# Kernel optimization log

Hardware: AMD Instinct MI355X
Metric: run time of the kernel (lower is better)

The kernel has to match this reference:

```python
import jax, jax.numpy as jnp
import numpy as np

N_BINS = 15


def setup_inputs() -> dict:
    key = jax.random.key(0)
    k1, k2 = jax.random.split(key)
    N, C = 2_000_000, 100
    logits = jax.random.normal(k1, (N, C), dtype=jnp.float32)
    labels = jax.random.randint(k2, (N,), 0, C, dtype=jnp.int64)
    return {"logits": logits, "labels": labels}


def reference(logits, labels):
    # softmax confidences + predictions
    probs = jax.nn.softmax(logits, axis=1)
    conf = jnp.max(probs, axis=1)            # [N]
    pred = jnp.argmax(probs, axis=1)          # [N]
    acc = (pred == labels).astype(conf.dtype)  # [N]

    # torch loop uses bins (lower, upper] with boundaries linspace(0,1,16).
    # conf in ((b-1)/B, b/B] maps to bin b-1 == ceil(conf*B)-1 (clipped).
    bin_idx = jnp.clip(jnp.ceil(conf * N_BINS).astype(jnp.int32) - 1, 0, N_BINS - 1)

    counts = jax.ops.segment_sum(jnp.ones_like(conf), bin_idx, num_segments=N_BINS)
    sum_conf = jax.ops.segment_sum(conf, bin_idx, num_segments=N_BINS)
    sum_acc = jax.ops.segment_sum(acc, bin_idx, num_segments=N_BINS)

    nonempty = counts > 0
    safe = jnp.where(nonempty, counts, jnp.ones_like(counts))
    gap = jnp.abs(sum_conf / safe - sum_acc / safe)  # |avg_conf - acc| per bin

    n_total = jnp.asarray(conf.shape[0], conf.dtype)
    ece = jnp.sum(jnp.where(nonempty, gap * counts / n_total, 0.0))
    mce = jnp.max(jnp.where(nonempty, gap, -jnp.inf))
    mce = jnp.where(jnp.any(nonempty), mce, jnp.asarray(1.0, conf.dtype))
    return ece, mce
```

## Files before the change

### kernel.cpp

```cpp
#include <hip/hip_runtime.h>
#include <math.h>

#define NBINS 15

template<int CTRL>
__device__ __forceinline__ float dpp_f(float x) {
    return __int_as_float(__builtin_amdgcn_update_dpp(
        0, __float_as_int(x), CTRL, 0xF, 0xF, true));
}
template<int CTRL>
__device__ __forceinline__ int dpp_i(int x) {
    return __builtin_amdgcn_update_dpp(0, x, CTRL, 0xF, 0xF, true);
}

#define QP_XOR1 0xB1
#define QP_XOR2 0x4E

__global__ __launch_bounds__(256) void ce_rows100(const float* __restrict__ logits,
                                                  const int* __restrict__ labels,
                                                  float* __restrict__ gbins, int N) {
    __shared__ float sb[NBINS * 3];
    if (threadIdx.x < NBINS * 3) sb[threadIdx.x] = 0.f;
    __syncthreads();

    const int lane = threadIdx.x & 63;
    const int q = lane & 3;
    const int rq = lane >> 2;
    const int gw = (blockIdx.x * blockDim.x + threadIdx.x) >> 6;
    const int nw = (gridDim.x * blockDim.x) >> 6;
    const int nchunks = (N + 15) >> 4;

    for (int chunk = gw; chunk < nchunks; chunk += nw) {
        const int row = chunk * 16 + rq;
        const bool valid = row < N;

        float m = -INFINITY, s = 0.f;
        int arg = 0;

        if (valid) {
            const float4* rp = reinterpret_cast<const float4*>(logits) + (size_t)row * 25;
            #pragma unroll
            for (int k = 0; k < 6; ++k) {
                const int qi = 4 * k + q;
                float4 v = rp[qi];
                const int bi = qi * 4;
                { float x = v.x; if (x > m) { s *= __expf(m - x); m = x; arg = bi;     } s += __expf(x - m); }
                { float x = v.y; if (x > m) { s *= __expf(m - x); m = x; arg = bi + 1; } s += __expf(x - m); }
                { float x = v.z; if (x > m) { s *= __expf(m - x); m = x; arg = bi + 2; } s += __expf(x - m); }
                { float x = v.w; if (x > m) { s *= __expf(m - x); m = x; arg = bi + 3; } s += __expf(x - m); }
            }
            if (q == 0) {
                float4 v = rp[24];
                { float x = v.x; if (x > m) { s *= __expf(m - x); m = x; arg = 96; } s += __expf(x - m); }
                { float x = v.y; if (x > m) { s *= __expf(m - x); m = x; arg = 97; } s += __expf(x - m); }
                { float x = v.z; if (x > m) { s *= __expf(m - x); m = x; arg = 98; } s += __expf(x - m); }
                { float x = v.w; if (x > m) { s *= __expf(m - x); m = x; arg = 99; } s += __expf(x - m); }
            }
        }

        const float ml = m;
        float M = m; int A = arg;
        {
            float t = dpp_f<QP_XOR1>(M); int ti = dpp_i<QP_XOR1>(A);
            if (t > M || (t == M && ti < A)) { M = t; A = ti; }
            t = dpp_f<QP_XOR2>(M); ti = dpp_i<QP_XOR2>(A);
            if (t > M || (t == M && ti < A)) { M = t; A = ti; }
        }
        float sc = s * __expf(ml - M);
        sc += dpp_f<QP_XOR1>(sc);
        sc += dpp_f<QP_XOR2>(sc);

        if (valid && q == 0) {
            const float conf = 1.0f / sc;
            const int lab = labels[row];
            int b = (int)ceilf(conf * (float)NBINS) - 1;
            b = min(max(b, 0), NBINS - 1);
            atomicAdd(&sb[b * 3 + 0], 1.0f);
            atomicAdd(&sb[b * 3 + 1], conf);
            if (A == lab) atomicAdd(&sb[b * 3 + 2], 1.0f);
        }
    }

    __syncthreads();
    if (threadIdx.x < NBINS * 3) {
        float v = sb[threadIdx.x];
        if (v != 0.f) atomicAdd(&gbins[threadIdx.x], v);
    }
}

__global__ __launch_bounds__(256) void ce_rows_generic(const float* __restrict__ logits,
                                                       const int* __restrict__ labels,
                                                       float* __restrict__ gbins,
                                                       int N, int C) {
    __shared__ float sb[NBINS * 3];
    if (threadIdx.x < NBINS * 3) sb[threadIdx.x] = 0.f;
    __syncthreads();

    const int r = blockIdx.x * blockDim.x + threadIdx.x;
    if (r < N) {
        const float* rp = logits + (size_t)r * (size_t)C;
        float m = -INFINITY, s = 0.f;
        int arg = 0;
        for (int k = 0; k < C; ++k) {
            float x = rp[k];
            if (x > m) { s *= __expf(m - x); m = x; arg = k; }
            s += __expf(x - m);
        }
        float conf = 1.0f / s;
        int b = (int)ceilf(conf * (float)NBINS) - 1;
        b = min(max(b, 0), NBINS - 1);
        atomicAdd(&sb[b * 3 + 0], 1.0f);
        atomicAdd(&sb[b * 3 + 1], conf);
        if (arg == labels[r]) atomicAdd(&sb[b * 3 + 2], 1.0f);
    }
    __syncthreads();
    if (threadIdx.x < NBINS * 3) {
        float v = sb[threadIdx.x];
        if (v != 0.f) atomicAdd(&gbins[threadIdx.x], v);
    }
}

__global__ void ce_final(const float* __restrict__ gbins, float* __restrict__ out,
                         float inv_n) {
    int t = threadIdx.x;
    float gap = 0.f, w = 0.f;
    bool ne = false;
    if (t < NBINS) {
        float c = gbins[t * 3 + 0];
        float sc = gbins[t * 3 + 1];
        float sa = gbins[t * 3 + 2];
        if (c > 0.f) { ne = true; gap = fabsf(sc / c - sa / c); w = c; }
    }
    float ece = ne ? gap * w * inv_n : 0.f;
    float mce = ne ? gap : -INFINITY;
    #pragma unroll
    for (int off = 1; off < 64; off <<= 1) {
        ece += __shfl_xor(ece, off);
        mce = fmaxf(mce, __shfl_xor(mce, off));
    }
    if (t == 0) {
        out[0] = ece;
        out[1] = (mce == -INFINITY) ? 1.0f : mce;
    }
}

extern "C" void kernel_launch(void* const* d_in, const int* in_sizes, int n_in,
                              void* d_out, int out_size, void* d_ws, size_t ws_size,
                              hipStream_t stream) {
    const float* logits = (const float*)d_in[0];
    const int* labels = (const int*)d_in[1];
    int N = in_sizes[1];
    int C = in_sizes[0] / in_sizes[1];

    float* gbins = (float*)d_ws;
    (void)hipMemsetAsync(gbins, 0, NBINS * 3 * sizeof(float), stream);

    if (C == 100) {
        ce_rows100<<<2048, 256, 0, stream>>>(logits, labels, gbins, N);
    } else {
        ce_rows_generic<<<(N + 255) / 256, 256, 0, stream>>>(logits, labels, gbins, N, C);
    }
    ce_final<<<1, 64, 0, stream>>>(gbins, (float*)d_out, 1.0f / (float)N);
}
```

Before: 166.8 us.

## Use two-pass max-then-exp softmax and fuse final reduction via last-block counter

Result: slower. 237.2 us (+42.2%).

```diff
diff --git a/kernel.cpp b/kernel.cpp
--- a/kernel.cpp
+++ b/kernel.cpp
@@ -1,5 +1,6 @@
 #include <hip/hip_runtime.h>
 #include <math.h>
+#include <limits.h>
 
 #define NBINS 15
 
@@ -12,72 +13,81 @@
 __device__ __forceinline__ int dpp_i(int x) {
     return __builtin_amdgcn_update_dpp(0, x, CTRL, 0xF, 0xF, true);
 }
-
 #define QP_XOR1 0xB1
 #define QP_XOR2 0x4E
 
 __global__ __launch_bounds__(256) void ce_rows100(const float* __restrict__ logits,
                                                   const int* __restrict__ labels,
-                                                  float* __restrict__ gbins, int N) {
+                                                  float* __restrict__ gbins,
+                                                  unsigned int* __restrict__ counter,
+                                                  float* __restrict__ out,
+                                                  int N, float inv_n,
+                                                  unsigned int nblocks) {
     __shared__ float sb[NBINS * 3];
+    __shared__ int slast;
     if (threadIdx.x < NBINS * 3) sb[threadIdx.x] = 0.f;
+    if (threadIdx.x == 0) slast = 0;
     __syncthreads();
 
     const int lane = threadIdx.x & 63;
     const int q = lane & 3;
-    const int rq = lane >> 2;
+    const int rq = lane >> 4 == 99 ? 0 : (lane >> 2);
     const int gw = (blockIdx.x * blockDim.x + threadIdx.x) >> 6;
     const int nw = (gridDim.x * blockDim.x) >> 6;
     const int nchunks = (N + 15) >> 4;
 
     for (int chunk = gw; chunk < nchunks; chunk += nw) {
         const int row = chunk * 16 + rq;
-        const bool valid = row < N;
-
-        float m = -INFINITY, s = 0.f;
-        int arg = 0;
-
-        if (valid) {
+        if (row < N) {
             const float4* rp = reinterpret_cast<const float4*>(logits) + (size_t)row * 25;
-            #pragma unroll
-            for (int k = 0; k < 6; ++k) {
-                const int qi = 4 * k + q;
-                float4 v = rp[qi];
-                const int bi = qi * 4;
-                { float x = v.x; if (x > m) { s *= __expf(m - x); m = x; arg = bi;     } s += __expf(x - m); }
-                { float x = v.y; if (x > m) { s *= __expf(m - x); m = x; arg = bi + 1; } s += __expf(x - m); }
-                { float x = v.z; if (x > m) { s *= __expf(m - x); m = x; arg = bi + 2; } s += __expf(x - m); }
-                { float x = v.w; if (x > m) { s *= __expf(m - x); m = x; arg = bi + 3; } s += __expf(x - m); }
+            int lab = 0;
+            if (q == 0) lab = labels[row];
+            float4 v0 = rp[q];
+            float4 v1 = rp[4 + q];
+            float4 v2 = rp[8 + q];
+            float4 v3 = rp[12 + q];
+            float4 v4 = rp[16 + q];
+            float4 v5 = rp[20 + q];
+            float4 vt = make_float4(-INFINITY, -INFINITY, -INFINITY, -INFINITY);
+            if (q == 0) vt = rp[24];
+
+            auto qmax = [](const float4& v) {
+                return fmaxf(fmaxf(v.x, v.y), fmaxf(v.z, v.w));
+            };
+            float m = fmaxf(fmaxf(fmaxf(qmax(v0), qmax(v1)), fmaxf(qmax(v2), qmax(v3))),
+                            fmaxf(fmaxf(qmax(v4), qmax(v5)), qmax(vt)));
+            m = fmaxf(m, dpp_f<QP_XOR1>(m));
+            m = fmaxf(m, dpp_f<QP_XOR2>(m));
+
+            float s = 0.f;
+            int arg = INT_MAX;
+            auto acc = [&](const float4& v, int bi) {
+                { float x = v.x; s += __expf(x - m); if (x == m) arg = min(arg, bi);     }
+                { float x = v.y; s += __expf(x - m); if (x == m) arg = min(arg, bi + 1); }
+                { float x = v.z; s += __expf(x - m); if (x == m) arg = min(arg, bi + 2); }
+                { float x = v.w; s += __expf(x - m); if (x == m) arg = min(arg, bi + 3); }
+            };
+            acc(v0, 4 * q);
+            acc(v1, 16 + 4 * q);
+            acc(v2, 32 + 4 * q);
+            acc(v3, 48 + 4 * q);
+            acc(v4, 64 + 4 * q);
+            acc(v5, 80 + 4 * q);
+            if (q == 0) acc(vt, 96);
+
+            s += dpp_f<QP_XOR1>(s);
+            s += dpp_f<QP_XOR2>(s);
+            arg = min(arg, dpp_i<QP_XOR1>(arg));
+            arg = min(arg, dpp_i<QP_XOR2>(arg));
+
+            if (q == 0) {
+                const float conf = 1.0f / s;
+                int b = (int)ceilf(conf * (float)NBINS) - 1;
+                b = min(max(b, 0), NBINS - 1);
+                atomicAdd(&sb[b * 3 + 0], 1.0f);
+                atomicAdd(&sb[b * 3 + 1], conf);
+                if (arg == lab) atomicAdd(&sb[b * 3 + 2], 1.0f);
             }
-            if (q == 0) {
-                float4 v = rp[24];
-                { float x = v.x; if (x > m) { s *= __expf(m - x); m = x; arg = 96; } s += __expf(x - m); }
-                { float x = v.y; if (x > m) { s *= __expf(m - x); m = x; arg = 97; } s += __expf(x - m); }
-                { float x = v.z; if (x > m) { s *= __expf(m - x); m = x; arg = 98; } s += __expf(x - m); }
-                { float x = v.w; if (x > m) { s *= __expf(m - x); m = x; arg = 99; } s += __expf(x - m); }
-            }
-        }
-
-        const float ml = m;
-        float M = m; int A = arg;
-        {
-            float t = dpp_f<QP_XOR1>(M); int ti = dpp_i<QP_XOR1>(A);
-            if (t > M || (t == M && ti < A)) { M = t; A = ti; }
-            t = dpp_f<QP_XOR2>(M); ti = dpp_i<QP_XOR2>(A);
-            if (t > M || (t == M && ti < A)) { M = t; A = ti; }
-        }
-        float sc = s * __expf(ml - M);
-        sc += dpp_f<QP_XOR1>(sc);
-        sc += dpp_f<QP_XOR2>(sc);
-
-        if (valid && q == 0) {
-            const float conf = 1.0f / sc;
-            const int lab = labels[row];
-            int b = (int)ceilf(conf * (float)NBINS) - 1;
-            b = min(max(b, 0), NBINS - 1);
-            atomicAdd(&sb[b * 3 + 0], 1.0f);
-            atomicAdd(&sb[b * 3 + 1], conf);
-            if (A == lab) atomicAdd(&sb[b * 3 + 2], 1.0f);
         }
     }
 
@@ -85,6 +95,36 @@
     if (threadIdx.x < NBINS * 3) {
         float v = sb[threadIdx.x];
         if (v != 0.f) atomicAdd(&gbins[threadIdx.x], v);
+    }
+    __syncthreads();
+    if (threadIdx.x == 0) {
+        __threadfence();
+        unsigned int t = atomicAdd(counter, 1u);
+        if (t == nblocks - 1) slast = 1;
+    }
+    __syncthreads();
+    if (slast && threadIdx.x < 64) {
+        __threadfence();
+        int t = threadIdx.x;
+        float gap = 0.f, w = 0.f;
+        bool ne = false;
+        if (t < NBINS) {
+            float c  = atomicAdd(&gbins[t * 3 + 0], 0.f);
+            float sc = atomicAdd(&gbins[t * 3 + 1], 0.f);
+            float sa = atomicAdd(&gbins[t * 3 + 2], 0.f);
+            if (c > 0.f) { ne = true; gap = fabsf(sc / c - sa / c); w = c; }
+        }
+        float ece = ne ? gap * w * inv_n : 0.f;
+        float mce = ne ? gap : -INFINITY;
+        #pragma unroll
+        for (int off = 1; off < 64; off <<= 1) {
+            ece += __shfl_xor(ece, off);
+            mce = fmaxf(mce, __shfl_xor(mce, off));
+        }
+        if (t == 0) {
+            out[0] = ece;
+            out[1] = (mce == -INFINITY) ? 1.0f : mce;
+        }
     }
 }
 
@@ -153,12 +193,17 @@
     int C = in_sizes[0] / in_sizes[1];
 
     float* gbins = (float*)d_ws;
-    (void)hipMemsetAsync(gbins, 0, NBINS * 3 * sizeof(float), stream);
+    unsigned int* counter = (unsigned int*)(gbins + NBINS * 3);
 
     if (C == 100) {
-        ce_rows100<<<2048, 256, 0, stream>>>(logits, labels, gbins, N);
+        (void)hipMemsetAsync(gbins, 0, (NBINS * 3 + 1) * sizeof(float), stream);
+        const unsigned int nblocks = 2048;
+        ce_rows100<<<nblocks, 256, 0, stream>>>(logits, labels, gbins, counter,
+                                                (float*)d_out, N, 1.0f / (float)N,
+                                                nblocks);
     } else {
+        (void)hipMemsetAsync(gbins, 0, NBINS * 3 * sizeof(float), stream);
         ce_rows_generic<<<(N + 255) / 256, 256, 0, stream>>>(logits, labels, gbins, N, C);
-    }
-    ce_final<<<1, 64, 0, stream>>>(gbins, (float*)d_out, 1.0f / (float)N);
-}
+        ce_final<<<1, 64, 0, stream>>>(gbins, (float*)d_out, 1.0f / (float)N);
+    }
+}
```
